# Kernel tuning notes

Measured on AMD Instinct MI355X. Metric: run time of the kernel, lower is better.

## Reference

```python
import jax, jax.numpy as jnp
import numpy as np

B, Cin, Cout, H, W = 8, 256, 256, 56, 56
KH, KW, PAD = 3, 3, 1
K = KH * KW
EPS = 1e-5


def _conv3x3(x, w, b):
    # x: [B,Cin,H,W], w: [O,Cin,3,3] -> [B,O,H,W] (stride 1, pad 1)
    y = jax.lax.conv_general_dilated(x, w, window_strides=(1, 1),
                                     padding=((PAD, PAD), (PAD, PAD)),
                                     dimension_numbers=('NCHW', 'OIHW', 'NCHW'))
    return y + b[None, :, None, None]


def _bilinear_gather(x, py, px):
    # x: [B,Cin,H,W]; py/px: [B,K,H,W] fractional sample coords (zero padding)
    y0 = jnp.floor(py); x0 = jnp.floor(px)
    ly = py - y0; lx = px - x0
    y0i = y0.astype(jnp.int32); x0i = x0.astype(jnp.int32)
    y1i = y0i + 1; x1i = x0i + 1
    xf = x.reshape(B, Cin, H * W)

    def corner(yi, xi, wgt):
        valid = ((yi >= 0) & (yi < H) & (xi >= 0) & (xi < W)).astype(x.dtype)
        idx = (jnp.clip(yi, 0, H - 1) * W + jnp.clip(xi, 0, W - 1)).reshape(B, K * H * W)
        v = jax.vmap(lambda xb, ib: xb[:, ib])(xf, idx)  # [B,Cin,K*H*W]
        v = v.reshape(B, Cin, K, H, W)
        return v * (wgt * valid)[:, None]

    return (corner(y0i, x0i, (1 - ly) * (1 - lx)) +
            corner(y0i, x1i, (1 - ly) * lx) +
            corner(y1i, x0i, ly * (1 - lx)) +
            corner(y1i, x1i, ly * lx))


def setup_inputs():
    key = jax.random.key(0)
    ks = jax.random.split(key, 4)
    x = jax.random.normal(ks[0], (B, Cin, H, W), jnp.float32)
    w_off = jax.random.normal(ks[1], (2 * K, Cin, KH, KW), jnp.float32) * 0.01
    b_off = jnp.zeros((2 * K,), jnp.float32)
    w_conv = jax.random.normal(ks[2], (Cout, Cin, KH, KW), jnp.float32) * (1.0 / np.sqrt(Cin * K))
    gamma = jnp.ones((Cout,), jnp.float32)
    beta = jnp.zeros((Cout,), jnp.float32)
    run_mean = jnp.zeros((Cout,), jnp.float32)
    run_var = jnp.ones((Cout,), jnp.float32)
    return {"x": x, "w_off": w_off, "b_off": b_off, "w_conv": w_conv,
            "gamma": gamma, "beta": beta, "run_mean": run_mean, "run_var": run_var}


def reference(x, w_off, b_off, w_conv, gamma, beta, run_mean, run_var):
    # 1) learned offsets: [B, 2K, H, W] -> [B, K, 2(y,x), H, W]
    off = _conv3x3(x, w_off, b_off).reshape(B, K, 2, H, W)
    dy, dx = off[:, :, 0], off[:, :, 1]
    ky = jnp.repeat(jnp.arange(KH, dtype=x.dtype), KW)  # [K]
    kx = jnp.tile(jnp.arange(KW, dtype=x.dtype), KH)
    py = jnp.arange(H, dtype=x.dtype)[None, None, :, None] - PAD + ky[None, :, None, None] + dy
    px = jnp.arange(W, dtype=x.dtype)[None, None, None, :] - PAD + kx[None, :, None, None] + dx
    # 2) bilinear gather -> [B, Cin, K, H, W]; 3) conv reduction over (Cin, K)
    val = _bilinear_gather(x, py, px)
    out = jnp.einsum('bikhw,oik->bohw', val, w_conv.reshape(Cout, Cin, K))
    # 4) BatchNorm (eval: running stats) + ReLU
    inv = gamma / jnp.sqrt(run_var + EPS)
    bn = (out - run_mean[None, :, None, None]) * inv[None, :, None, None] + beta[None, :, None, None]
    return jnp.maximum(bn, 0.0)
```

## Files before the change

### kernel.cpp

```cpp
#include <hip/hip_runtime.h>


#define BATCH 8
#define CIN   256
#define COUT  256
#define HH    56
#define WW    56
#define HW    3136
#define NPIX  25088
#define KTAP  9
#define KG    2304
#define NKT   36

typedef unsigned short ushortT;
typedef _Float16 f16x8 __attribute__((ext_vector_type(8)));
typedef float f32x4 __attribute__((ext_vector_type(4)));

__device__ __forceinline__ f16x8 lds_ldh8(const ushortT* p) {
    uint4 u = *(const uint4*)p;
    return __builtin_bit_cast(f16x8, u);
}
__device__ __forceinline__ unsigned packh2(float v0, float v1) {
    _Float16 h0 = (_Float16)v0, h1 = (_Float16)v1;
    return (unsigned)__builtin_bit_cast(unsigned short, h0)
         | ((unsigned)__builtin_bit_cast(unsigned short, h1) << 16);
}

#define KA_NT 1568
#define KA_NW 2594

__global__ __launch_bounds__(256) void kA_prep(
    const float* __restrict__ x, float* __restrict__ xt,
    const float* __restrict__ wconv, const float* __restrict__ woff,
    const float* __restrict__ g, const float* __restrict__ be,
    const float* __restrict__ rm, const float* __restrict__ rv,
    ushortT* __restrict__ Ah, ushortT* __restrict__ A0h,
    float* __restrict__ scale, float* __restrict__ shift)
{
    __shared__ float t[64][65];
    const int tid = threadIdx.x;
    if (blockIdx.x < KA_NT) {
        const int bid = (blockIdx.x & 7) * 196 + (blockIdx.x >> 3);
        const int b   = bid / 196;
        const int r   = bid % 196;
        const int hw0 = (r >> 2) * 64;
        const int c0  = (r & 3) * 64;
        {
            const int c_l = tid >> 2, ch = (tid & 3) * 16;
            const float* src = x + ((size_t)(b*CIN + c0 + c_l))*HW + hw0 + ch;
            float4 v0 = *(const float4*)(src + 0);
            float4 v1 = *(const float4*)(src + 4);
            float4 v2 = *(const float4*)(src + 8);
            float4 v3 = *(const float4*)(src + 12);
            *(float4*)&t[c_l][ch + 0]  = v0;
            *(float4*)&t[c_l][ch + 4]  = v1;
            *(float4*)&t[c_l][ch + 8]  = v2;
            *(float4*)&t[c_l][ch + 12] = v3;
        }
        __syncthreads();
        {
            const int hw_l = tid >> 2, cc = (tid & 3) * 16;
            float* dst = xt + ((size_t)(b*HW + hw0 + hw_l))*CIN + c0 + cc;
            #pragma unroll
            for (int q = 0; q < 4; ++q) {
                float4 o;
                o.x = t[cc + q*4 + 0][hw_l];
                o.y = t[cc + q*4 + 1][hw_l];
                o.z = t[cc + q*4 + 2][hw_l];
                o.w = t[cc + q*4 + 3][hw_l];
                *(float4*)(dst + q*4) = o;
            }
        }
    } else {
        const int id = (blockIdx.x - KA_NT)*256 + tid;
        if (id < COUT*KG) {
            int m = id / KG, kg = id % KG;
            int k = kg >> 8, i = kg & 255;
            float f = wconv[(m*CIN + i)*9 + k];
            int kt = kg >> 6, kk = kg & 63;
            _Float16 h = (_Float16)f;
            Ah[kt*16384 + m*64 + (kk ^ ((m & 7) << 3))] = __builtin_bit_cast(unsigned short, h);
        } else if (id < COUT*KG + 32*KG) {
            int id2 = id - COUT*KG;
            int m = id2 / KG, kg = id2 % KG;
            int k = kg >> 8, i = kg & 255;
            float f = (m < 18) ? woff[(m*CIN + i)*9 + k] : 0.f;
            int kt = kg >> 6, kk = kg & 63;
            _Float16 h = (_Float16)f;
            A0h[kt*2048 + m*64 + (kk ^ ((m & 7) << 3))] = __builtin_bit_cast(unsigned short, h);
        } else if (id < COUT*KG + 32*KG + 256) {
            int c = id - (COUT*KG + 32*KG);
            float inv = g[c] / sqrtf(rv[c] + 1e-5f);
            scale[c] = inv;
            shift[c] = be[c] - rm[c]*inv;
        }
    }
}

__global__ __launch_bounds__(256, 4) void k1_offmfma(
    const float* __restrict__ xt, const ushortT* __restrict__ A0h_g,
    const float* __restrict__ b_off, float* __restrict__ off)
{
    __shared__ __align__(16) ushortT A0[32*64];
    __shared__ __align__(16) ushortT Bh[2][64*64];

    const int tid = threadIdx.x;
    const int x8 = blockIdx.x & 7;
    const int lt = blockIdx.x >> 3;
    const int bn0 = (x8*49 + lt) * 64;

    const int wv = tid >> 6, lane = tid & 63;
    const int l16 = lane & 15, lq = lane >> 4;
    const int px_l = tid >> 2, g2 = tid & 3;

    const int hw = lt*64 + px_l;
    const int h = hw / WW, w = hw % WW;

    f32x4 acc[2] = {};
    float4 iv0, iv1, iv2, iv3;

    #define K1_IM2COL(ktg_) do {                                               \
        const int tap_ = (ktg_) >> 2, ic_ = (ktg_) & 3;                        \
        const int ky_ = tap_ / 3 - 1, kx_ = tap_ % 3 - 1;                      \
        const int hs_ = h + ky_, ws_ = w + kx_;                                \
        const bool valid_ = (hs_ >= 0 && hs_ < HH && ws_ >= 0 && ws_ < WW);    \
        const int hc_ = min(max(hs_, 0), HH-1), wc_ = min(max(ws_, 0), WW-1);  \
        const float* p_ = xt + ((size_t)(x8*HW + hc_*WW + wc_))*CIN + ic_*64 + g2*16; \
        iv0 = *(const float4*)(p_ + 0);  iv1 = *(const float4*)(p_ + 4);       \
        iv2 = *(const float4*)(p_ + 8);  iv3 = *(const float4*)(p_ + 12);      \
        if (!valid_) {                                                         \
            iv0 = iv1 = iv2 = iv3 = make_float4(0.f, 0.f, 0.f, 0.f);           \
        }                                                                      \
    } while (0)

    #define K1_PACK(buf_) do {                                                 \
        uint4 h0_, h1_;                                                        \
        h0_.x = packh2(iv0.x, iv0.y); h0_.y = packh2(iv0.z, iv0.w);            \
        h0_.z = packh2(iv1.x, iv1.y); h0_.w = packh2(iv1.z, iv1.w);            \
        h1_.x = packh2(iv2.x, iv2.y); h1_.y = packh2(iv2.z, iv2.w);            \
        h1_.z = packh2(iv3.x, iv3.y); h1_.w = packh2(iv3.z, iv3.w);            \
        const int base_ = g2 * 16;                                             \
        *(uint4*)&Bh[buf_][px_l*64 + ((base_ + 0) ^ ((px_l & 7) << 3))] = h0_; \
        *(uint4*)&Bh[buf_][px_l*64 + ((base_ + 8) ^ ((px_l & 7) << 3))] = h1_; \
    } while (0)

    #define K1_ISSUE_A0(ktg_)                                                  \
        __builtin_amdgcn_global_load_lds(                                      \
            (const __attribute__((address_space(1))) unsigned*)((const char*)A0h_g + (ktg_)*4096 + tid*16), \
            (__attribute__((address_space(3))) unsigned*)((char*)A0 + wv*1024), 16, 0, 0)

    K1_IM2COL(0);
    K1_ISSUE_A0(0);
    K1_PACK(0);
    asm volatile("s_waitcnt lgkmcnt(0)" ::: "memory");
    __builtin_amdgcn_s_barrier();

    for (int t = 0; t < NKT; ++t) {
        const int cur = t & 1;
        if (t + 1 < NKT) {
            K1_IM2COL(t + 1);
            asm volatile("s_waitcnt vmcnt(4)" ::: "memory");
        } else {
            asm volatile("s_waitcnt vmcnt(0)" ::: "memory");
        }
        __builtin_amdgcn_s_barrier();
        __builtin_amdgcn_sched_barrier(0);
        {
            __builtin_amdgcn_s_setprio(1);
            #pragma unroll
            for (int ks = 0; ks < 2; ++ks) {
                const int kk0 = ks*32 + lq*8;
                const int m0 = l16, m1 = 16 + l16;
                f16x8 a0 = lds_ldh8(&A0[m0*64 + (kk0 ^ ((m0 & 7) << 3))]);
                f16x8 a1 = lds_ldh8(&A0[m1*64 + (kk0 ^ ((m1 & 7) << 3))]);
                const int n = wv*16 + l16;
                f16x8 b0 = lds_ldh8(&Bh[cur][n*64 + (kk0 ^ ((n & 7) << 3))]);
                acc[0] = __builtin_amdgcn_mfma_f32_16x16x32_f16(a0, b0, acc[0], 0, 0, 0);
                acc[1] = __builtin_amdgcn_mfma_f32_16x16x32_f16(a1, b0, acc[1], 0, 0, 0);
            }
            __builtin_amdgcn_s_setprio(0);
        }
        if (t + 1 < NKT) K1_PACK(cur ^ 1);
        asm volatile("s_waitcnt lgkmcnt(0)" ::: "memory");
        __builtin_amdgcn_s_barrier();
        if (t + 1 < NKT) K1_ISSUE_A0(t + 1);
    }

    const int hw2 = lt*64 + wv*16 + l16;
    #pragma unroll
    for (int mf = 0; mf < 2; ++mf) {
        #pragma unroll
        for (int r = 0; r < 4; ++r) {
            const int m = mf*16 + lq*4 + r;
            if (m < 18)
                off[((size_t)x8*18 + m)*HW + hw2] = acc[mf][r] + b_off[m];
        }
    }
    #undef K1_IM2COL
    #undef K1_PACK
    #undef K1_ISSUE_A0
}

__global__ __launch_bounds__(512, 4) void k3_main(
    const float* __restrict__ xt, const float* __restrict__ off_g,
    const ushortT* __restrict__ Ah_g, const float* __restrict__ scale_g,
    const float* __restrict__ shift_g, float* __restrict__ out)
{
    __shared__ __align__(16) ushortT Ah_t[256*64];
    __shared__ __align__(16) ushortT Bh_t[2][64*64];
    __shared__ __align__(16) ushortT Bl_t[2][64*64];
    __shared__ float s_scale[256], s_shift[256];

    const int tid = threadIdx.x;
    const int bimg = blockIdx.x & 7;
    const int lt   = blockIdx.x >> 3;
    if (tid < 256) { s_scale[tid] = scale_g[tid]; s_shift[tid] = shift_g[tid]; }

    const int wv = tid >> 6, lane = tid & 63;
    const int l16 = lane & 15, lq = lane >> 4;
    const int mbase = (wv >> 1) * 64;
    const int nbase = (wv & 1) * 32;
    const int px_l = tid >> 3, g = tid & 7;
    const int hwp  = lt*64 + px_l;
    const int hp   = hwp / WW, wp = hwp % WW;

    int   mi[4];
    float mwv[4];
    f32x4 Gc[4][2];
    f32x4 acc[4][2] = {};

    #define META(tap_) do {                                                    \
        float dy_ = off_g[((size_t)bimg*18 + 2*(tap_)    )*HW + hwp];          \
        float dx_ = off_g[((size_t)bimg*18 + 2*(tap_) + 1)*HW + hwp];          \
        float py_ = (float)(hp - 1 + ((tap_) / 3)) + dy_;                      \
        float px_ = (float)(wp - 1 + ((tap_) % 3)) + dx_;                      \
        py_ = fminf(fmaxf(py_, -30000.f), 30000.f);                            \
        px_ = fminf(fmaxf(px_, -30000.f), 30000.f);                            \
        float y0f_ = floorf(py_), x0f_ = floorf(px_);                          \
        int y0_ = (int)y0f_, x0_ = (int)x0f_;                                  \
        float ly_ = py_ - y0f_, lx_ = px_ - x0f_;                              \
        float wy0_ = 1.f - ly_, wx0_ = 1.f - lx_;                              \
        _Pragma("unroll")                                                      \
        for (int c_ = 0; c_ < 4; ++c_) {                                       \
            int yi_ = y0_ + (c_ >> 1), xi_ = x0_ + (c_ & 1);                   \
            bool v_ = (yi_ >= 0) && (yi_ < HH) && (xi_ >= 0) && (xi_ < WW);    \
            int yc_ = min(max(yi_, 0), HH-1), xc_ = min(max(xi_, 0), WW-1);    \
            mi[c_] = (bimg*HW + yc_*WW + xc_)*CIN;                             \
            float wy_ = (c_ >> 1) ? ly_ : wy0_;                                \
            float wx_ = (c_ & 1) ? lx_ : wx0_;                                 \
            mwv[c_] = v_ ? wy_*wx_ : 0.f;                                      \
        }                                                                      \
    } while (0)

    #define ISSUE_GATHER(j_) do {                                              \
        const float* base_ = xt + ((j_) & 3)*64 + g*8;                         \
        _Pragma("unroll")                                                      \
        for (int c_ = 0; c_ < 4; ++c_) {                                       \
            const float* p_ = base_ + mi[c_];                                  \
            Gc[c_][0] = *(const f32x4*)p_;                                     \
            Gc[c_][1] = *(const f32x4*)(p_ + 4);                               \
        }                                                                      \
    } while (0)

    #define BLEND_WRITE(buf_) do {                                             \
        float v_[8];                                                           \
        _Pragma("unroll")                                                      \
        for (int q_ = 0; q_ < 4; ++q_) {                                       \
            v_[q_]   = mwv[0]*Gc[0][0][q_] + mwv[1]*Gc[1][0][q_]               \
                     + mwv[2]*Gc[2][0][q_] + mwv[3]*Gc[3][0][q_];              \
            v_[4+q_] = mwv[0]*Gc[0][1][q_] + mwv[1]*Gc[1][1][q_]               \
                     + mwv[2]*Gc[2][1][q_] + mwv[3]*Gc[3][1][q_];              \
        }                                                                      \
        uint4 hi_, lo_;                                                        \
        float r_[8];                                                           \
        _Pragma("unroll")                                                      \
        for (int q_ = 0; q_ < 8; ++q_) {                                       \
            _Float16 hh_ = (_Float16)v_[q_];                                   \
            r_[q_] = v_[q_] - (float)hh_;                                      \
        }                                                                      \
        hi_.x = packh2(v_[0], v_[1]); hi_.y = packh2(v_[2], v_[3]);            \
        hi_.z = packh2(v_[4], v_[5]); hi_.w = packh2(v_[6], v_[7]);            \
        lo_.x = packh2(r_[0], r_[1]); lo_.y = packh2(r_[2], r_[3]);            \
        lo_.z = packh2(r_[4], r_[5]); lo_.w = packh2(r_[6], r_[7]);            \
        const int idx_ = px_l*64 + ((g*8) ^ ((px_l & 7) << 3));                \
        *(uint4*)&Bh_t[buf_][idx_] = hi_;                                      \
        *(uint4*)&Bl_t[buf_][idx_] = lo_;                                      \
    } while (0)

    #define ISSUE_A(j_) do {                                                   \
        const char* gs_ = (const char*)Ah_g + (size_t)(j_)*32768;              \
        _Pragma("unroll")                                                      \
        for (int it_ = 0; it_ < 4; ++it_)                                      \
            __builtin_amdgcn_global_load_lds(                                  \
                (const __attribute__((address_space(1))) unsigned*)(gs_ + it_*8192 + tid*16), \
                (__attribute__((address_space(3))) unsigned*)((char*)Ah_t + it_*8192 + wv*1024), \
                16, 0, 0);                                                     \
    } while (0)

    #define MFMA_PHASE(cur_) do {                                              \
        __builtin_amdgcn_s_setprio(1);                                         \
        _Pragma("unroll")                                                      \
        for (int ks_ = 0; ks_ < 2; ++ks_) {                                    \
            const int kk0_ = ks_*32 + lq*8;                                    \
            f16x8 a_[4], bh_[2], bl_[2];                                       \
            _Pragma("unroll")                                                  \
            for (int mf_ = 0; mf_ < 4; ++mf_) {                                \
                const int m_ = mbase + mf_*16 + l16;                           \
                a_[mf_] = lds_ldh8(&Ah_t[m_*64 + (kk0_ ^ ((m_ & 7) << 3))]);   \
            }                                                                  \
            _Pragma("unroll")                                                  \
            for (int nf_ = 0; nf_ < 2; ++nf_) {                                \
                const int n_ = nbase + nf_*16 + l16;                           \
                const int ix_ = n_*64 + (kk0_ ^ ((n_ & 7) << 3));              \
                bh_[nf_] = lds_ldh8(&Bh_t[cur_][ix_]);                         \
                bl_[nf_] = lds_ldh8(&Bl_t[cur_][ix_]);                         \
            }                                                                  \
            _Pragma("unroll")                                                  \
            for (int mf_ = 0; mf_ < 4; ++mf_) {                                \
                _Pragma("unroll")                                              \
                for (int nf_ = 0; nf_ < 2; ++nf_) {                            \
                    acc[mf_][nf_] = __builtin_amdgcn_mfma_f32_16x16x32_f16(a_[mf_], bh_[nf_], acc[mf_][nf_], 0, 0, 0); \
                    acc[mf_][nf_] = __builtin_amdgcn_mfma_f32_16x16x32_f16(a_[mf_], bl_[nf_], acc[mf_][nf_], 0, 0, 0); \
                }                                                              \
            }                                                                  \
        }                                                                      \
        __builtin_amdgcn_s_setprio(0);                                         \
    } while (0)

    META(0);
    ISSUE_GATHER(0);
    ISSUE_A(0);
    BLEND_WRITE(0);
    asm volatile("s_waitcnt lgkmcnt(0)" ::: "memory");
    __builtin_amdgcn_s_barrier();

    for (int kt = 0; kt < NKT; ++kt) {
        const int cur = kt & 1;
        if (kt + 1 < NKT) {
            if (((kt + 1) & 3) == 0) META((kt + 1) >> 2);
            ISSUE_GATHER(kt + 1);
            asm volatile("s_waitcnt vmcnt(8)" ::: "memory");
        } else {
            asm volatile("s_waitcnt vmcnt(0)" ::: "memory");
        }
        __builtin_amdgcn_s_barrier();
        __builtin_amdgcn_sched_barrier(0);
        MFMA_PHASE(cur);
        if (kt + 1 < NKT) BLEND_WRITE(cur ^ 1);
        asm volatile("s_waitcnt lgkmcnt(0)" ::: "memory");
        __builtin_amdgcn_s_barrier();
        if (kt + 1 < NKT) ISSUE_A(kt + 1);
    }

    const int hwb = lt * 64;
    #pragma unroll
    for (int mf = 0; mf < 4; ++mf) {
        #pragma unroll
        for (int nf = 0; nf < 2; ++nf) {
            const int hwloc = hwb + nbase + nf*16 + l16;
            const int m0 = mbase + mf*16 + lq*4;
            float* op = out + ((size_t)bimg*COUT + m0)*HW + hwloc;
            const f32x4 v = acc[mf][nf];
            #pragma unroll
            for (int r = 0; r < 4; ++r) {
                float val = fmaxf(v[r]*s_scale[m0 + r] + s_shift[m0 + r], 0.f);
                op[(size_t)r*HW] = val;
            }
        }
    }
    #undef META
    #undef ISSUE_GATHER
    #undef BLEND_WRITE
    #undef ISSUE_A
    #undef MFMA_PHASE
}

extern "C" void kernel_launch(void* const* d_in, const int* in_sizes, int n_in,
                              void* d_out, int out_size, void* d_ws, size_t ws_size,
                              hipStream_t stream)
{
    const float* x      = (const float*)d_in[0];
    const float* w_off  = (const float*)d_in[1];
    const float* b_off  = (const float*)d_in[2];
    const float* w_conv = (const float*)d_in[3];
    const float* gamma  = (const float*)d_in[4];
    const float* beta   = (const float*)d_in[5];
    const float* rmean  = (const float*)d_in[6];
    const float* rvar   = (const float*)d_in[7];
    float* out = (float*)d_out;
    char* ws = (char*)d_ws;

    float*   xt    = (float*)(ws + 0);
    float*   off   = (float*)(ws + 25690112);
    ushortT* Ah    = (ushortT*)(ws + 27496448);
    ushortT* A0h   = (ushortT*)(ws + 28676096);
    float*   scale = (float*)(ws + 28823552);
    float*   shift = (float*)(ws + 28824576);

    hipLaunchKernelGGL(kA_prep, dim3(KA_NT + KA_NW), dim3(256), 0, stream,
                       x, xt, w_conv, w_off, gamma, beta, rmean, rvar,
                       Ah, A0h, scale, shift);
    hipLaunchKernelGGL(k1_offmfma, dim3(392), dim3(256), 0, stream, xt, A0h, b_off, off);
    hipLaunchKernelGGL(k3_main, dim3(392), dim3(512), 0, stream,
                       xt, off, Ah, scale, shift, out);
}
```

Before: 214.4 us.

## Drop hi/lo fp16 split in main GEMM, halve pixel tile, split-K offset conv

The main deformable-conv kernel no longer splits the blended samples into high and low fp16 halves, so it runs half as many MFMAs and LDS writes per tile. The pixel tile per block is halved from 64 to 32, which doubles the grid to 784 blocks, and launch bounds are raised for higher occupancy. The offset-conv kernel moves to 512 threads: its two K-halves are split across wave groups and combined through LDS at the end. Dropping the residual term loses precision in the B operand, which may push the result past the accuracy tolerance, and the smaller tile means the weight tile in LDS is reloaded for fewer pixels.

```diff
diff --git a/kernel.cpp b/kernel.cpp
--- a/kernel.cpp
+++ b/kernel.cpp
@@ -97,7 +97,7 @@
     }
 }
 
-__global__ __launch_bounds__(256, 4) void k1_offmfma(
+__global__ __launch_bounds__(512, 4) void k1_offmfma(
     const float* __restrict__ xt, const ushortT* __restrict__ A0h_g,
     const float* __restrict__ b_off, float* __restrict__ off)
 {
@@ -107,17 +107,18 @@
     const int tid = threadIdx.x;
     const int x8 = blockIdx.x & 7;
     const int lt = blockIdx.x >> 3;
-    const int bn0 = (x8*49 + lt) * 64;
 
     const int wv = tid >> 6, lane = tid & 63;
     const int l16 = lane & 15, lq = lane >> 4;
-    const int px_l = tid >> 2, g2 = tid & 3;
+    const int wn = wv & 3;
+    const int ksw = wv >> 2;
+    const int px_l = tid >> 3, g2 = tid & 7;
 
     const int hw = lt*64 + px_l;
     const int h = hw / WW, w = hw % WW;
 
     f32x4 acc[2] = {};
-    float4 iv0, iv1, iv2, iv3;
+    float4 iv0, iv1;
 
     #define K1_IM2COL(ktg_) do {                                               \
         const int tap_ = (ktg_) >> 2, ic_ = (ktg_) & 3;                        \
@@ -125,23 +126,18 @@
         const int hs_ = h + ky_, ws_ = w + kx_;                                \
         const bool valid_ = (hs_ >= 0 && hs_ < HH && ws_ >= 0 && ws_ < WW);    \
         const int hc_ = min(max(hs_, 0), HH-1), wc_ = min(max(ws_, 0), WW-1);  \
-        const float* p_ = xt + ((size_t)(x8*HW + hc_*WW + wc_))*CIN + ic_*64 + g2*16; \
+        const float* p_ = xt + ((size_t)(x8*HW + hc_*WW + wc_))*CIN + ic_*64 + g2*8; \
         iv0 = *(const float4*)(p_ + 0);  iv1 = *(const float4*)(p_ + 4);       \
-        iv2 = *(const float4*)(p_ + 8);  iv3 = *(const float4*)(p_ + 12);      \
         if (!valid_) {                                                         \
-            iv0 = iv1 = iv2 = iv3 = make_float4(0.f, 0.f, 0.f, 0.f);           \
+            iv0 = iv1 = make_float4(0.f, 0.f, 0.f, 0.f);                       \
         }                                                                      \
     } while (0)
 
     #define K1_PACK(buf_) do {                                                 \
-        uint4 h0_, h1_;                                                        \
+        uint4 h0_;                                                             \
         h0_.x = packh2(iv0.x, iv0.y); h0_.y = packh2(iv0.z, iv0.w);            \
         h0_.z = packh2(iv1.x, iv1.y); h0_.w = packh2(iv1.z, iv1.w);            \
-        h1_.x = packh2(iv2.x, iv2.y); h1_.y = packh2(iv2.z, iv2.w);            \
-        h1_.z = packh2(iv3.x, iv3.y); h1_.w = packh2(iv3.z, iv3.w);            \
-        const int base_ = g2 * 16;                                             \
-        *(uint4*)&Bh[buf_][px_l*64 + ((base_ + 0) ^ ((px_l & 7) << 3))] = h0_; \
-        *(uint4*)&Bh[buf_][px_l*64 + ((base_ + 8) ^ ((px_l & 7) << 3))] = h1_; \
+        *(uint4*)&Bh[buf_][px_l*64 + ((g2*8) ^ ((px_l & 7) << 3))] = h0_;      \
     } while (0)
 
     #define K1_ISSUE_A0(ktg_)                                                  \
@@ -150,7 +146,7 @@
             (__attribute__((address_space(3))) unsigned*)((char*)A0 + wv*1024), 16, 0, 0)
 
     K1_IM2COL(0);
-    K1_ISSUE_A0(0);
+    if (tid < 256) K1_ISSUE_A0(0);
     K1_PACK(0);
     asm volatile("s_waitcnt lgkmcnt(0)" ::: "memory");
     __builtin_amdgcn_s_barrier();
@@ -159,7 +155,7 @@
         const int cur = t & 1;
         if (t + 1 < NKT) {
             K1_IM2COL(t + 1);
-            asm volatile("s_waitcnt vmcnt(4)" ::: "memory");
+            asm volatile("s_waitcnt vmcnt(2)" ::: "memory");
         } else {
             asm volatile("s_waitcnt vmcnt(0)" ::: "memory");
         }
@@ -167,33 +163,43 @@
         __builtin_amdgcn_sched_barrier(0);
         {
             __builtin_amdgcn_s_setprio(1);
-            #pragma unroll
-            for (int ks = 0; ks < 2; ++ks) {
-                const int kk0 = ks*32 + lq*8;
-                const int m0 = l16, m1 = 16 + l16;
-                f16x8 a0 = lds_ldh8(&A0[m0*64 + (kk0 ^ ((m0 & 7) << 3))]);
-                f16x8 a1 = lds_ldh8(&A0[m1*64 + (kk0 ^ ((m1 & 7) << 3))]);
-                const int n = wv*16 + l16;
-                f16x8 b0 = lds_ldh8(&Bh[cur][n*64 + (kk0 ^ ((n & 7) << 3))]);
-                acc[0] = __builtin_amdgcn_mfma_f32_16x16x32_f16(a0, b0, acc[0], 0, 0, 0);
-                acc[1] = __builtin_amdgcn_mfma_f32_16x16x32_f16(a1, b0, acc[1], 0, 0, 0);
-            }
+            const int kk0 = ksw*32 + lq*8;
+            const int m0 = l16, m1 = 16 + l16;
+            f16x8 a0 = lds_ldh8(&A0[m0*64 + (kk0 ^ ((m0 & 7) << 3))]);
+            f16x8 a1 = lds_ldh8(&A0[m1*64 + (kk0 ^ ((m1 & 7) << 3))]);
+            const int n = wn*16 + l16;
+            f16x8 b0 = lds_ldh8(&Bh[cur][n*64 + (kk0 ^ ((n & 7) << 3))]);
+            acc[0] = __builtin_amdgcn_mfma_f32_16x16x32_f16(a0, b0, acc[0], 0, 0, 0);
+            acc[1] = __builtin_amdgcn_mfma_f32_16x16x32_f16(a1, b0, acc[1], 0, 0, 0);
             __builtin_amdgcn_s_setprio(0);
         }
         if (t + 1 < NKT) K1_PACK(cur ^ 1);
         asm volatile("s_waitcnt lgkmcnt(0)" ::: "memory");
         __builtin_amdgcn_s_barrier();
-        if (t + 1 < NKT) K1_ISSUE_A0(t + 1);
-    }
-
-    const int hw2 = lt*64 + wv*16 + l16;
-    #pragma unroll
-    for (int mf = 0; mf < 2; ++mf) {
-        #pragma unroll
-        for (int r = 0; r < 4; ++r) {
-            const int m = mf*16 + lq*4 + r;
-            if (m < 18)
-                off[((size_t)x8*18 + m)*HW + hw2] = acc[mf][r] + b_off[m];
+        if (t + 1 < NKT && tid < 256) K1_ISSUE_A0(t + 1);
+    }
+
+    {
+        float* red = (float*)&Bh[0][0];
+        if (wv >= 4) {
+            const int sl = tid - 256;
+            *(f32x4*)&red[sl*8 + 0] = acc[0];
+            *(f32x4*)&red[sl*8 + 4] = acc[1];
+        }
+        __syncthreads();
+        if (wv < 4) {
+            acc[0] += *(const f32x4*)&red[tid*8 + 0];
+            acc[1] += *(const f32x4*)&red[tid*8 + 4];
+            const int hw2 = lt*64 + wn*16 + l16;
+            #pragma unroll
+            for (int mf = 0; mf < 2; ++mf) {
+                #pragma unroll
+                for (int r = 0; r < 4; ++r) {
+                    const int m = mf*16 + lq*4 + r;
+                    if (m < 18)
+                        off[((size_t)x8*18 + m)*HW + hw2] = acc[mf][r] + b_off[m];
+                }
+            }
         }
     }
     #undef K1_IM2COL
@@ -201,14 +207,13 @@
     #undef K1_ISSUE_A0
 }
 
-__global__ __launch_bounds__(512, 4) void k3_main(
+__global__ __launch_bounds__(512, 6) void k3_main(
     const float* __restrict__ xt, const float* __restrict__ off_g,
     const ushortT* __restrict__ Ah_g, const float* __restrict__ scale_g,
     const float* __restrict__ shift_g, float* __restrict__ out)
 {
     __shared__ __align__(16) ushortT Ah_t[256*64];
-    __shared__ __align__(16) ushortT Bh_t[2][64*64];
-    __shared__ __align__(16) ushortT Bl_t[2][64*64];
+    __shared__ __align__(16) ushortT Bh_t[2][32*64];
     __shared__ float s_scale[256], s_shift[256];
 
     const int tid = threadIdx.x;
@@ -219,15 +224,15 @@
     const int wv = tid >> 6, lane = tid & 63;
     const int l16 = lane & 15, lq = lane >> 4;
     const int mbase = (wv >> 1) * 64;
-    const int nbase = (wv & 1) * 32;
-    const int px_l = tid >> 3, g = tid & 7;
-    const int hwp  = lt*64 + px_l;
+    const int nbase = (wv & 1) * 16;
+    const int px_l = tid >> 4, g = tid & 15;
+    const int hwp  = lt*32 + px_l;
     const int hp   = hwp / WW, wp = hwp % WW;
 
     int   mi[4];
     float mwv[4];
-    f32x4 Gc[4][2];
-    f32x4 acc[4][2] = {};
+    f32x4 Gc[4];
+    f32x4 acc[4] = {};
 
     #define META(tap_) do {                                                    \
         float dy_ = off_g[((size_t)bimg*18 + 2*(tap_)    )*HW + hwp];          \
@@ -253,38 +258,21 @@
     } while (0)
 
     #define ISSUE_GATHER(j_) do {                                              \
-        const float* base_ = xt + ((j_) & 3)*64 + g*8;                         \
+        const float* base_ = xt + ((j_) & 3)*64 + g*4;                         \
         _Pragma("unroll")                                                      \
-        for (int c_ = 0; c_ < 4; ++c_) {                                       \
-            const float* p_ = base_ + mi[c_];                                  \
-            Gc[c_][0] = *(const f32x4*)p_;                                     \
-            Gc[c_][1] = *(const f32x4*)(p_ + 4);                               \
-        }                                                                      \
+        for (int c_ = 0; c_ < 4; ++c_)                                         \
+            Gc[c_] = *(const f32x4*)(base_ + mi[c_]);                          \
     } while (0)
 
     #define BLEND_WRITE(buf_) do {                                             \
-        float v_[8];                                                           \
-        _Pragma("unroll")                                                      \
-        for (int q_ = 0; q_ < 4; ++q_) {                                       \
-            v_[q_]   = mwv[0]*Gc[0][0][q_] + mwv[1]*Gc[1][0][q_]               \
-                     + mwv[2]*Gc[2][0][q_] + mwv[3]*Gc[3][0][q_];              \
-            v_[4+q_] = mwv[0]*Gc[0][1][q_] + mwv[1]*Gc[1][1][q_]               \
-                     + mwv[2]*Gc[2][1][q_] + mwv[3]*Gc[3][1][q_];              \
-        }                                                                      \
-        uint4 hi_, lo_;                                                        \
-        float r_[8];                                                           \
-        _Pragma("unroll")                                                      \
-        for (int q_ = 0; q_ < 8; ++q_) {                                       \
-            _Float16 hh_ = (_Float16)v_[q_];                                   \
-            r_[q_] = v_[q_] - (float)hh_;                                      \
-        }                                                                      \
-        hi_.x = packh2(v_[0], v_[1]); hi_.y = packh2(v_[2], v_[3]);            \
-        hi_.z = packh2(v_[4], v_[5]); hi_.w = packh2(v_[6], v_[7]);            \
-        lo_.x = packh2(r_[0], r_[1]); lo_.y = packh2(r_[2], r_[3]);            \
-        lo_.z = packh2(r_[4], r_[5]); lo_.w = packh2(r_[6], r_[7]);            \
-        const int idx_ = px_l*64 + ((g*8) ^ ((px_l & 7) << 3));                \
-        *(uint4*)&Bh_t[buf_][idx_] = hi_;                                      \
-        *(uint4*)&Bl_t[buf_][idx_] = lo_;                                      \
+        float v0_ = mwv[0]*Gc[0][0] + mwv[1]*Gc[1][0] + mwv[2]*Gc[2][0] + mwv[3]*Gc[3][0]; \
+        float v1_ = mwv[0]*Gc[0][1] + mwv[1]*Gc[1][1] + mwv[2]*Gc[2][1] + mwv[3]*Gc[3][1]; \
+        float v2_ = mwv[0]*Gc[0][2] + mwv[1]*Gc[1][2] + mwv[2]*Gc[2][2] + mwv[3]*Gc[3][2]; \
+        float v3_ = mwv[0]*Gc[0][3] + mwv[1]*Gc[1][3] + mwv[2]*Gc[2][3] + mwv[3]*Gc[3][3]; \
+        uint2 u_;                                                              \
+        u_.x = packh2(v0_, v1_);  u_.y = packh2(v2_, v3_);                     \
+        const int idx_ = px_l*64 + ((g*4) ^ ((px_l & 7) << 3));                \
+        *(uint2*)&Bh_t[buf_][idx_] = u_;                                       \
     } while (0)
 
     #define ISSUE_A(j_) do {                                                   \
@@ -302,27 +290,19 @@
         _Pragma("unroll")                                                      \
         for (int ks_ = 0; ks_ < 2; ++ks_) {                                    \
             const int kk0_ = ks_*32 + lq*8;                                    \
-            f16x8 a_[4], bh_[2], bl_[2];                                       \
+            f16x8 a_[4], b_;                                                   \
             _Pragma("unroll")                                                  \
             for (int mf_ = 0; mf_ < 4; ++mf_) {                                \
                 const int m_ = mbase + mf_*16 + l16;                           \
                 a_[mf_] = lds_ldh8(&Ah_t[m_*64 + (kk0_ ^ ((m_ & 7) << 3))]);   \
             }                                                                  \
-            _Pragma("unroll")                                                  \
-            for (int nf_ = 0; nf_ < 2; ++nf_) {                                \
-                const int n_ = nbase + nf_*16 + l16;                           \
-                const int ix_ = n_*64 + (kk0_ ^ ((n_ & 7) << 3));              \
-                bh_[nf_] = lds_ldh8(&Bh_t[cur_][ix_]);                         \
-                bl_[nf_] = lds_ldh8(&Bl_t[cur_][ix_]);                         \
+            {                                                                  \
+                const int n_ = nbase + l16;                                    \
+                b_ = lds_ldh8(&Bh_t[cur_][n_*64 + (kk0_ ^ ((n_ & 7) << 3))]);  \
             }                                                                  \
             _Pragma("unroll")                                                  \
-            for (int mf_ = 0; mf_ < 4; ++mf_) {                                \
-                _Pragma("unroll")                                              \
-                for (int nf_ = 0; nf_ < 2; ++nf_) {                            \
-                    acc[mf_][nf_] = __builtin_amdgcn_mfma_f32_16x16x32_f16(a_[mf_], bh_[nf_], acc[mf_][nf_], 0, 0, 0); \
-                    acc[mf_][nf_] = __builtin_amdgcn_mfma_f32_16x16x32_f16(a_[mf_], bl_[nf_], acc[mf_][nf_], 0, 0, 0); \
-                }                                                              \
-            }                                                                  \
+            for (int mf_ = 0; mf_ < 4; ++mf_)                                  \
+                acc[mf_] = __builtin_amdgcn_mfma_f32_16x16x32_f16(a_[mf_], b_, acc[mf_], 0, 0, 0); \
         }                                                                      \
         __builtin_amdgcn_s_setprio(0);                                         \
     } while (0)
@@ -337,9 +317,14 @@
     for (int kt = 0; kt < NKT; ++kt) {
         const int cur = kt & 1;
         if (kt + 1 < NKT) {
-            if (((kt + 1) & 3) == 0) META((kt + 1) >> 2);
-            ISSUE_GATHER(kt + 1);
-            asm volatile("s_waitcnt vmcnt(8)" ::: "memory");
+            if (((kt + 1) & 3) == 0) {
+                META((kt + 1) >> 2);
+                ISSUE_GATHER(kt + 1);
+                asm volatile("s_waitcnt vmcnt(6)" ::: "memory");
+            } else {
+                ISSUE_GATHER(kt + 1);
+                asm volatile("s_waitcnt vmcnt(4)" ::: "memory");
+            }
         } else {
             asm volatile("s_waitcnt vmcnt(0)" ::: "memory");
         }
@@ -352,20 +337,16 @@
         if (kt + 1 < NKT) ISSUE_A(kt + 1);
     }
 
-    const int hwb = lt * 64;
+    const int hwloc = lt*32 + nbase + l16;
     #pragma unroll
     for (int mf = 0; mf < 4; ++mf) {
+        const int m0 = mbase + mf*16 + lq*4;
+        float* op = out + ((size_t)bimg*COUT + m0)*HW + hwloc;
+        const f32x4 v = acc[mf];
         #pragma unroll
-        for (int nf = 0; nf < 2; ++nf) {
-            const int hwloc = hwb + nbase + nf*16 + l16;
-            const int m0 = mbase + mf*16 + lq*4;
-            float* op = out + ((size_t)bimg*COUT + m0)*HW + hwloc;
-            const f32x4 v = acc[mf][nf];
-            #pragma unroll
-            for (int r = 0; r < 4; ++r) {
-                float val = fmaxf(v[r]*s_scale[m0 + r] + s_shift[m0 + r], 0.f);
-                op[(size_t)r*HW] = val;
-            }
+        for (int r = 0; r < 4; ++r) {
+            float val = fmaxf(v[r]*s_scale[m0 + r] + s_shift[m0 + r], 0.f);
+            op[(size_t)r*HW] = val;
         }
     }
     #undef META
@@ -400,7 +381,7 @@
     hipLaunchKernelGGL(kA_prep, dim3(KA_NT + KA_NW), dim3(256), 0, stream,
                        x, xt, w_conv, w_off, gamma, beta, rmean, rvar,
                        Ah, A0h, scale, shift);
-    hipLaunchKernelGGL(k1_offmfma, dim3(392), dim3(256), 0, stream, xt, A0h, b_off, off);
-    hipLaunchKernelGGL(k3_main, dim3(392), dim3(512), 0, stream,
+    hipLaunchKernelGGL(k1_offmfma, dim3(392), dim3(512), 0, stream, xt, A0h, b_off, off);
+    hipLaunchKernelGGL(k3_main, dim3(784), dim3(512), 0, stream,
                        xt, off, Ah, scale, shift, out);
 }
```

Measured after the change: 221.1 us. 3.1% more time.
